# Kernel optimization log

Measured on AMD Instinct MI355X. Metric: run time of the kernel, lower is better.

## Reference

```python
import jax, jax.numpy as jnp
import numpy as np

EPS = 1e-5  # torch LayerNorm default

def layernorm(x, gamma, beta):
    mu = jnp.mean(x, axis=-1, keepdims=True)
    var = jnp.mean(jnp.square(x - mu), axis=-1, keepdims=True)
    return (x - mu) * jax.lax.rsqrt(var + EPS) * gamma + beta

def setup_inputs() -> dict:
    key = jax.random.key(0)
    ks = jax.random.split(key, 8)
    B, S, D = 4, 2048, 1024
    s = 1.0 / np.sqrt(D)  # torch Linear init scale
    return {
        "x": jax.random.normal(ks[0], (B, S, D), dtype=jnp.float32),
        "Wq": jax.random.uniform(ks[1], (D, D), jnp.float32, -s, s),
        "bq": jax.random.uniform(ks[2], (D,), jnp.float32, -s, s),
        "Wk": jax.random.uniform(ks[3], (D, D), jnp.float32, -s, s),
        "bk": jax.random.uniform(ks[4], (D,), jnp.float32, -s, s),
        "Wv": jax.random.uniform(ks[5], (D, D), jnp.float32, -s, s),
        "bv": jax.random.uniform(ks[6], (D,), jnp.float32, -s, s),
        "gamma": jnp.ones((D,), jnp.float32),
        "beta": jnp.zeros((D,), jnp.float32),
    }

def reference(x, Wq, bq, Wk, bk, Wv, bv, gamma, beta):
    # torch Linear: x @ W.T + b; shared LayerNorm applied to each projection
    q = layernorm(jnp.einsum('bsd,ed->bse', x, Wq) + bq, gamma, beta)
    k = layernorm(jnp.einsum('bsd,ed->bse', x, Wk) + bk, gamma, beta)
    v = layernorm(jnp.einsum('bsd,ed->bse', x, Wv) + bv, gamma, beta)
    att = jnp.einsum('bqd,bkd->bqk', q, k)  # no 1/sqrt(d) scaling in original
    att = jax.nn.softmax(att, axis=-1)
    # dropout is identity in eval mode (reference baseline)
    return jnp.einsum('bqk,bkd->bqd', att, v)
```

## Files before the change

kernel.cpp:

```cpp
#include <hip/hip_runtime.h>

typedef _Float16 f16;
typedef __attribute__((ext_vector_type(4))) _Float16 f16x4;
typedef __attribute__((ext_vector_type(8))) _Float16 f16x8;
typedef __attribute__((ext_vector_type(4))) float f32x4;

#define GLB_AS __attribute__((address_space(1)))
#define LDS_AS __attribute__((address_space(3)))

__device__ __forceinline__ void async_copy16(const void* g, void* l) {
  __builtin_amdgcn_global_load_lds((const GLB_AS void*)g, (LDS_AS void*)l, 16, 0, 0);
}

template <typename OutT, int MODE, bool BIAS>
__global__ __launch_bounds__(256) void gemm_kn(
    const f16* __restrict__ A, const f16* __restrict__ B, OutT* __restrict__ C,
    int lda, int ldb, int ldc, int K, long sA, long sB, long sC,
    int tiles_x, int tiles_y,
    const float* __restrict__ b0, const float* __restrict__ b1,
    const float* __restrict__ b2)
{
  constexpr int BM = 128, BK = 32;
  __shared__ __align__(16) f16 Ash[2][BM * BK];
  __shared__ __align__(16) f16 Bsh[2][BM * BK];

  int bx, by, bz;
  {
    const int n = blockIdx.x;
    if (MODE == 0) {
      by = n % tiles_y;
      const int r = n / tiles_y;
      bx = r % tiles_x;
      bz = r / tiles_x;
    } else {
      const int j = n & 7, i = n >> 3;
      bz = j >> 1;
      bx = i >> 3;
      by = (j & 1) * 8 + (i & 7);
    }
  }

  A += (long)bz * sA;
  B += (long)bz * sB;
  C += (long)bz * sC;

  const int tid  = threadIdx.x;
  const int wave = tid >> 6, lane = tid & 63;
  const int m0 = by * BM, n0 = bx * BM;
  const int wm = (wave >> 1) * 64, wn = (wave & 1) * 64;
  const int r16 = lane & 15, quad = lane >> 4;

  const int srow = wave * 32 + (lane >> 2);
  const int skb  = (lane & 3) * 8;
  const f16* Ag = A + (long)(m0 + srow) * lda + skb;
  const f16* Bg = B + (long)(n0 + srow) * ldb + skb;
  const int lo0 = (wave * 32) * BK;
  const int lo1 = (wave * 32 + 16) * BK;

  async_copy16(Ag,                  &Ash[0][lo0]);
  async_copy16(Ag + 16 * (long)lda, &Ash[0][lo1]);
  async_copy16(Bg,                  &Bsh[0][lo0]);
  async_copy16(Bg + 16 * (long)ldb, &Bsh[0][lo1]);

  f32x4 acc[4][4] = {};

  int buf = 0;
  for (int k0 = 0; k0 < K; k0 += BK, buf ^= 1) {
    __syncthreads();

    if (k0 + BK < K) {
      const int nb = buf ^ 1;
      const long k1 = k0 + BK;
      async_copy16(Ag + k1,                  &Ash[nb][lo0]);
      async_copy16(Ag + k1 + 16 * (long)lda, &Ash[nb][lo1]);
      async_copy16(Bg + k1,                  &Bsh[nb][lo0]);
      async_copy16(Bg + k1 + 16 * (long)ldb, &Bsh[nb][lo1]);
    }

    f16x8 af[4], bf[4];
#pragma unroll
    for (int i = 0; i < 4; i++) {
      af[i] = *(const f16x8*)&Ash[buf][(wm + i * 16 + r16) * BK + quad * 8];
      bf[i] = *(const f16x8*)&Bsh[buf][(wn + i * 16 + r16) * BK + quad * 8];
    }
#pragma unroll
    for (int i = 0; i < 4; i++)
#pragma unroll
      for (int j = 0; j < 4; j++)
        acc[i][j] = __builtin_amdgcn_mfma_f32_16x16x32_f16(af[i], bf[j], acc[i][j], 0, 0, 0);
  }

  float bias_j[4] = {0.f, 0.f, 0.f, 0.f};
  if (BIAS) {
    const float* bias = (bz == 0) ? b0 : (bz == 1) ? b1 : b2;
#pragma unroll
    for (int j = 0; j < 4; j++) bias_j[j] = bias[n0 + wn + j * 16 + r16];
  }
#pragma unroll
  for (int i = 0; i < 4; i++)
#pragma unroll
    for (int j = 0; j < 4; j++)
#pragma unroll
      for (int r = 0; r < 4; r++) {
        long row = m0 + wm + i * 16 + quad * 4 + r;
        long col = n0 + wn + j * 16 + r16;
        C[row * (long)ldc + col] = (OutT)(acc[i][j][r] + bias_j[j]);
      }
}

__global__ __launch_bounds__(256) void cast_all(
    const float* __restrict__ x, const float* __restrict__ Wq,
    const float* __restrict__ Wk, const float* __restrict__ Wv,
    f16* __restrict__ Xh, f16* __restrict__ Wh)
{
  const long off = (long)blockIdx.x * 1024 + threadIdx.x * 4;
  const float* src;
  f16* dst;
  if (off < 8388608L) {
    src = x + off;
    dst = Xh + off;
  } else {
    const long o = off - 8388608L;
    src = (o < 1048576L) ? Wq + o
        : (o < 2097152L) ? Wk + (o - 1048576L)
                         : Wv + (o - 2097152L);
    dst = Wh + o;
  }
  const float4 v = *(const float4*)src;
  f16x4 h;
  h.x = (f16)v.x; h.y = (f16)v.y; h.z = (f16)v.z; h.w = (f16)v.w;
  *(f16x4*)dst = h;
}

__global__ __launch_bounds__(256) void ln_kernel(
    f16* __restrict__ P, const float* __restrict__ gamma,
    const float* __restrict__ beta)
{
  f16* p = P + (long)blockIdx.y * 8388608 + (long)blockIdx.x * 1024;
  const int tid = threadIdx.x;
  const int e = tid * 4;

  f16x4 raw = *(const f16x4*)(p + e);
  float v0 = (float)raw.x, v1 = (float)raw.y;
  float v2 = (float)raw.z, v3 = (float)raw.w;
  float s  = v0 + v1 + v2 + v3;
  float s2 = v0 * v0 + v1 * v1 + v2 * v2 + v3 * v3;

#pragma unroll
  for (int off = 32; off > 0; off >>= 1) {
    s  += __shfl_down(s, off, 64);
    s2 += __shfl_down(s2, off, 64);
  }
  __shared__ float red[10];
  const int wave = tid >> 6, lane = tid & 63;
  if (lane == 0) { red[wave] = s; red[4 + wave] = s2; }
  __syncthreads();
  if (tid == 0) {
    red[8] = red[0] + red[1] + red[2] + red[3];
    red[9] = red[4] + red[5] + red[6] + red[7];
  }
  __syncthreads();
  const float mu   = red[8] * (1.f / 1024.f);
  const float var  = red[9] * (1.f / 1024.f) - mu * mu;
  const float rstd = rsqrtf(var + 1e-5f);

  float4 gg = *(const float4*)(gamma + e);
  float4 be = *(const float4*)(beta + e);
  f16x4 o;
  o.x = (f16)((v0 - mu) * rstd * gg.x + be.x);
  o.y = (f16)((v1 - mu) * rstd * gg.y + be.y);
  o.z = (f16)((v2 - mu) * rstd * gg.z + be.z);
  o.w = (f16)((v3 - mu) * rstd * gg.w + be.w);
  *(f16x4*)(p + e) = o;
}

__global__ __launch_bounds__(256) void transpose_kernel(const f16* __restrict__ V,
                                                        f16* __restrict__ Vt)
{
  const int S = 2048, D = 1024;
  const f16* v = V + (long)blockIdx.z * ((long)S * D);
  f16* vt = Vt + (long)blockIdx.z * ((long)D * S);
  __shared__ f16 tile[64][66];
  const int d0 = blockIdx.x * 64, j0 = blockIdx.y * 64;
  const int tx = threadIdx.x & 63, ty = threadIdx.x >> 6;
#pragma unroll
  for (int r = ty; r < 64; r += 4)
    tile[r][tx] = v[(long)(j0 + r) * D + d0 + tx];
  __syncthreads();
#pragma unroll
  for (int r = ty; r < 64; r += 4)
    vt[(long)(d0 + r) * S + j0 + tx] = tile[tx][r];
}

__global__ __launch_bounds__(256) void softmax_kernel(float* __restrict__ Sc)
{
  float* srow = Sc + (long)blockIdx.x * 2048;
  const int tid = threadIdx.x;
  float4 a = ((const float4*)srow)[tid];
  float4 b = ((const float4*)srow)[256 + tid];

  float m = fmaxf(fmaxf(fmaxf(a.x, a.y), fmaxf(a.z, a.w)),
                  fmaxf(fmaxf(b.x, b.y), fmaxf(b.z, b.w)));
#pragma unroll
  for (int off = 32; off > 0; off >>= 1) m = fmaxf(m, __shfl_down(m, off, 64));
  __shared__ float red[6];
  const int wave = tid >> 6, lane = tid & 63;
  if (lane == 0) red[wave] = m;
  __syncthreads();
  if (tid == 0) red[4] = fmaxf(fmaxf(red[0], red[1]), fmaxf(red[2], red[3]));
  __syncthreads();
  const float M = red[4];

  a.x = __expf(a.x - M); a.y = __expf(a.y - M);
  a.z = __expf(a.z - M); a.w = __expf(a.w - M);
  b.x = __expf(b.x - M); b.y = __expf(b.y - M);
  b.z = __expf(b.z - M); b.w = __expf(b.w - M);
  float s = a.x + a.y + a.z + a.w + b.x + b.y + b.z + b.w;
#pragma unroll
  for (int off = 32; off > 0; off >>= 1) s += __shfl_down(s, off, 64);
  if (lane == 0) red[wave] = s;
  __syncthreads();
  if (tid == 0) red[5] = red[0] + red[1] + red[2] + red[3];
  __syncthreads();
  const float inv = 1.0f / red[5];

  f16* orow = (f16*)srow;
  f16x4 oa, ob;
  oa.x = (f16)(a.x * inv); oa.y = (f16)(a.y * inv);
  oa.z = (f16)(a.z * inv); oa.w = (f16)(a.w * inv);
  ob.x = (f16)(b.x * inv); ob.y = (f16)(b.y * inv);
  ob.z = (f16)(b.z * inv); ob.w = (f16)(b.w * inv);
  ((f16x4*)orow)[tid]       = oa;
  ((f16x4*)orow)[256 + tid] = ob;
}

extern "C" void kernel_launch(void* const* d_in, const int* in_sizes, int n_in,
                              void* d_out, int out_size, void* d_ws, size_t ws_size,
                              hipStream_t stream)
{
  const float* x     = (const float*)d_in[0];
  const float* Wq    = (const float*)d_in[1];
  const float* bq    = (const float*)d_in[2];
  const float* Wk    = (const float*)d_in[3];
  const float* bk    = (const float*)d_in[4];
  const float* Wv    = (const float*)d_in[5];
  const float* bv    = (const float*)d_in[6];
  const float* gamma = (const float*)d_in[7];
  const float* beta  = (const float*)d_in[8];
  float* out = (float*)d_out;

  char* ws = (char*)d_ws;
  f16*   P  = (f16*)(ws);
  f16*   Vt = (f16*)(ws + (48u << 20));
  float* Sc = (float*)(ws + (64u << 20));
  f16*   Xh = (f16*)(ws + (64u << 20));
  f16*   Wh = (f16*)(ws + (80u << 20));

  cast_all<<<11264, 256, 0, stream>>>(x, Wq, Wk, Wv, Xh, Wh);

  gemm_kn<f16, 0, true><<<1536, 256, 0, stream>>>(
      Xh, Wh, P, 1024, 1024, 1024, 1024, 0L, 1048576L, 8388608L,
      8, 64, bq, bk, bv);

  ln_kernel<<<dim3(8192, 3), 256, 0, stream>>>(P, gamma, beta);

  transpose_kernel<<<dim3(16, 32, 4), 256, 0, stream>>>(P + 2L * 8388608, Vt);

  gemm_kn<float, 1, false><<<1024, 256, 0, stream>>>(
      P, P + 8388608, Sc, 1024, 1024, 2048, 1024, 2097152L, 2097152L, 4194304L,
      16, 16, nullptr, nullptr, nullptr);

  softmax_kernel<<<8192, 256, 0, stream>>>(Sc);

  gemm_kn<float, 1, false><<<512, 256, 0, stream>>>(
      (const f16*)Sc, Vt, out, 4096, 2048, 1024, 2048, 8388608L, 2097152L, 2097152L,
      8, 16, nullptr, nullptr, nullptr);
}
```

Before: 315.5 us.

## Replace GEMM with 8-wave, 4-stage pipelined kernel using larger tiles and swizzled LDS

Replaces the 256-thread, double-buffered 128x128 GEMM with a 512-thread kernel that uses 128x256 or 256x256 tiles. It keeps a 4-deep async global-to-LDS pipeline with explicit vmcnt waits, XOR-swizzles the LDS chunks to avoid bank conflicts, and splits each k-step into two halves. Each half interleaves the next stage's loads with the MFMA work under setprio and sched barriers. The aim is to hide global load latency, raise data reuse per tile and cut LDS conflicts in all three GEMMs. In exchange there are far fewer blocks per GEMM (256 for two of them), more LDS and register pressure, and hand-tuned waitcnt logic that is easy to get wrong.

New measurement: 305.0 us. 3.3% less time.

```diff
diff --git a/kernel.cpp b/kernel.cpp
--- a/kernel.cpp
+++ b/kernel.cpp
@@ -12,17 +12,38 @@
   __builtin_amdgcn_global_load_lds((const GLB_AS void*)g, (LDS_AS void*)l, 16, 0, 0);
 }
 
-template <typename OutT, int MODE, bool BIAS>
-__global__ __launch_bounds__(256) void gemm_kn(
+#define WAITVM(N) asm volatile("s_waitcnt vmcnt(" #N ")" ::: "memory")
+#define WAITLGKM0() asm volatile("s_waitcnt lgkmcnt(0)" ::: "memory")
+
+#define STAGE_A(t_) do {                                                     \
+    const int _b = (t_) & 3; const long _k = (long)(t_) * 32;                \
+    async_copy16(Ag + _k, &Ash[_b][sl]);                                     \
+    if constexpr (IA == 2)                                                   \
+      async_copy16(Ag + _k + 128l * lda, &Ash[_b][sl + 128 * 32]);           \
+  } while (0)
+#define STAGE_B(t_) do {                                                     \
+    const int _b = (t_) & 3; const long _k = (long)(t_) * 32;                \
+    async_copy16(Bg + _k, &Bsh[_b][sl]);                                     \
+    if constexpr (IB == 2)                                                   \
+      async_copy16(Bg + _k + 128l * ldb, &Bsh[_b][sl + 128 * 32]);           \
+  } while (0)
+
+template <int BM, int BN, typename OutT, int MODE, bool BIAS>
+__global__ __launch_bounds__(512, 2) void gemm8p(
     const f16* __restrict__ A, const f16* __restrict__ B, OutT* __restrict__ C,
     int lda, int ldb, int ldc, int K, long sA, long sB, long sC,
     int tiles_x, int tiles_y,
     const float* __restrict__ b0, const float* __restrict__ b1,
     const float* __restrict__ b2)
 {
-  constexpr int BM = 128, BK = 32;
-  __shared__ __align__(16) f16 Ash[2][BM * BK];
-  __shared__ __align__(16) f16 Bsh[2][BM * BK];
+  constexpr int BK = 32;
+  constexpr int WM = BM / 2, WN = BN / 4;
+  constexpr int RM = WM / 16, RN = WN / 16;
+  constexpr int IA = BM / 128, IB = BN / 128;
+  constexpr int IT = IA + IB;
+
+  __shared__ __align__(16) f16 Ash[4][BM * BK];
+  __shared__ __align__(16) f16 Bsh[4][BN * BK];
 
   int bx, by, bz;
   {
@@ -33,10 +54,10 @@
       bx = r % tiles_x;
       bz = r / tiles_x;
     } else {
-      const int j = n & 7, i = n >> 3;
+      const int j = n & 7, i = n >> 3, th = tiles_y >> 1;
       bz = j >> 1;
-      bx = i >> 3;
-      by = (j & 1) * 8 + (i & 7);
+      bx = i / th;
+      by = (j & 1) * th + i % th;
     }
   }
 
@@ -46,64 +67,124 @@
 
   const int tid  = threadIdx.x;
   const int wave = tid >> 6, lane = tid & 63;
-  const int m0 = by * BM, n0 = bx * BM;
-  const int wm = (wave >> 1) * 64, wn = (wave & 1) * 64;
+  const int wr = wave >> 2, wc = wave & 3;
+  const int m0 = by * BM, n0 = bx * BN;
   const int r16 = lane & 15, quad = lane >> 4;
 
-  const int srow = wave * 32 + (lane >> 2);
-  const int skb  = (lane & 3) * 8;
-  const f16* Ag = A + (long)(m0 + srow) * lda + skb;
-  const f16* Bg = B + (long)(n0 + srow) * ldb + skb;
-  const int lo0 = (wave * 32) * BK;
-  const int lo1 = (wave * 32 + 16) * BK;
-
-  async_copy16(Ag,                  &Ash[0][lo0]);
-  async_copy16(Ag + 16 * (long)lda, &Ash[0][lo1]);
-  async_copy16(Bg,                  &Bsh[0][lo0]);
-  async_copy16(Bg + 16 * (long)ldb, &Bsh[0][lo1]);
-
-  f32x4 acc[4][4] = {};
-
-  int buf = 0;
-  for (int k0 = 0; k0 < K; k0 += BK, buf ^= 1) {
-    __syncthreads();
-
-    if (k0 + BK < K) {
-      const int nb = buf ^ 1;
-      const long k1 = k0 + BK;
-      async_copy16(Ag + k1,                  &Ash[nb][lo0]);
-      async_copy16(Ag + k1 + 16 * (long)lda, &Ash[nb][lo1]);
-      async_copy16(Bg + k1,                  &Bsh[nb][lo0]);
-      async_copy16(Bg + k1 + 16 * (long)ldb, &Bsh[nb][lo1]);
+  const int srow = wave * 16 + (lane >> 2);
+  const int schunk = ((lane & 3) ^ ((lane >> 3) & 3)) * 8;
+  const f16* Ag = A + (long)(m0 + srow) * lda + schunk;
+  const f16* Bg = B + (long)(n0 + srow) * ldb + schunk;
+  const int sl = (wave * 16) * BK;
+
+  const int NT = K / BK;
+
+  STAGE_A(0); STAGE_B(0);
+  STAGE_A(1); STAGE_B(1);
+  STAGE_A(2); STAGE_B(2);
+
+  f32x4 acc[RM][RN] = {};
+
+  const int rchunk = (quad ^ ((r16 >> 1) & 3)) * 8;
+  const int rdA = (wr * WM + r16) * BK + rchunk;
+  const int rdB = (wc * WN + r16) * BK + rchunk;
+
+  for (int t = 0; t < NT; ++t) {
+    if constexpr (IT == 4) {
+      if (t < NT - 2) { WAITVM(8); } else if (t == NT - 2) { WAITVM(4); } else { WAITVM(0); }
+    } else {
+      if (t < NT - 2) { WAITVM(6); } else if (t == NT - 2) { WAITVM(3); } else { WAITVM(0); }
     }
-
-    f16x8 af[4], bf[4];
-#pragma unroll
-    for (int i = 0; i < 4; i++) {
-      af[i] = *(const f16x8*)&Ash[buf][(wm + i * 16 + r16) * BK + quad * 8];
-      bf[i] = *(const f16x8*)&Bsh[buf][(wn + i * 16 + r16) * BK + quad * 8];
+    __builtin_amdgcn_s_barrier();
+
+    const f16* As = Ash[t & 3];
+    const f16* Bs = Bsh[t & 3];
+    f16x8 af[4], bf[RN];
+
+    if constexpr (RM == 8) {
+#pragma unroll
+      for (int j = 0; j < RN; j++) bf[j] = *(const f16x8*)&Bs[rdB + j * 16 * BK];
+#pragma unroll
+      for (int i = 0; i < 4; i++) af[i] = *(const f16x8*)&As[rdA + i * 16 * BK];
+      if (t + 3 < NT) STAGE_A(t + 3);
+      __builtin_amdgcn_s_barrier();
+      WAITLGKM0();
+      __builtin_amdgcn_sched_barrier(0);
+      __builtin_amdgcn_s_setprio(1);
+#pragma unroll
+      for (int i = 0; i < 4; i++)
+#pragma unroll
+        for (int j = 0; j < RN; j++)
+          acc[i][j] = __builtin_amdgcn_mfma_f32_16x16x32_f16(af[i], bf[j], acc[i][j], 0, 0, 0);
+      __builtin_amdgcn_s_setprio(0);
+      __builtin_amdgcn_sched_barrier(0);
+      __builtin_amdgcn_s_barrier();
+      f16x8 af1[4];
+#pragma unroll
+      for (int i = 0; i < 4; i++) af1[i] = *(const f16x8*)&As[rdA + (4 + i) * 16 * BK];
+      if (t + 3 < NT) STAGE_B(t + 3);
+      __builtin_amdgcn_s_barrier();
+      WAITLGKM0();
+      __builtin_amdgcn_sched_barrier(0);
+      __builtin_amdgcn_s_setprio(1);
+#pragma unroll
+      for (int i = 0; i < 4; i++)
+#pragma unroll
+        for (int j = 0; j < RN; j++)
+          acc[4 + i][j] = __builtin_amdgcn_mfma_f32_16x16x32_f16(af1[i], bf[j], acc[4 + i][j], 0, 0, 0);
+      __builtin_amdgcn_s_setprio(0);
+      __builtin_amdgcn_sched_barrier(0);
+    } else {
+#pragma unroll
+      for (int i = 0; i < 4; i++) af[i] = *(const f16x8*)&As[rdA + i * 16 * BK];
+#pragma unroll
+      for (int j = 0; j < 2; j++) bf[j] = *(const f16x8*)&Bs[rdB + j * 16 * BK];
+      if (t + 3 < NT) STAGE_A(t + 3);
+      __builtin_amdgcn_s_barrier();
+      WAITLGKM0();
+      __builtin_amdgcn_sched_barrier(0);
+      __builtin_amdgcn_s_setprio(1);
+#pragma unroll
+      for (int i = 0; i < 4; i++)
+#pragma unroll
+        for (int j = 0; j < 2; j++)
+          acc[i][j] = __builtin_amdgcn_mfma_f32_16x16x32_f16(af[i], bf[j], acc[i][j], 0, 0, 0);
+      __builtin_amdgcn_s_setprio(0);
+      __builtin_amdgcn_sched_barrier(0);
+      __builtin_amdgcn_s_barrier();
+#pragma unroll
+      for (int j = 2; j < 4; j++) bf[j] = *(const f16x8*)&Bs[rdB + j * 16 * BK];
+      if (t + 3 < NT) STAGE_B(t + 3);
+      __builtin_amdgcn_s_barrier();
+      WAITLGKM0();
+      __builtin_amdgcn_sched_barrier(0);
+      __builtin_amdgcn_s_setprio(1);
+#pragma unroll
+      for (int i = 0; i < 4; i++)
+#pragma unroll
+        for (int j = 2; j < 4; j++)
+          acc[i][j] = __builtin_amdgcn_mfma_f32_16x16x32_f16(af[i], bf[j], acc[i][j], 0, 0, 0);
+      __builtin_amdgcn_s_setprio(0);
+      __builtin_amdgcn_sched_barrier(0);
     }
-#pragma unroll
-    for (int i = 0; i < 4; i++)
-#pragma unroll
-      for (int j = 0; j < 4; j++)
-        acc[i][j] = __builtin_amdgcn_mfma_f32_16x16x32_f16(af[i], bf[j], acc[i][j], 0, 0, 0);
-  }
-
-  float bias_j[4] = {0.f, 0.f, 0.f, 0.f};
-  if (BIAS) {
+  }
+
+  float bias_j[RN];
+#pragma unroll
+  for (int j = 0; j < RN; j++) bias_j[j] = 0.f;
+  if constexpr (BIAS) {
     const float* bias = (bz == 0) ? b0 : (bz == 1) ? b1 : b2;
 #pragma unroll
-    for (int j = 0; j < 4; j++) bias_j[j] = bias[n0 + wn + j * 16 + r16];
-  }
-#pragma unroll
-  for (int i = 0; i < 4; i++)
-#pragma unroll
-    for (int j = 0; j < 4; j++)
+    for (int j = 0; j < RN; j++) bias_j[j] = bias[n0 + wc * WN + j * 16 + r16];
+  }
+#pragma unroll
+  for (int i = 0; i < RM; i++)
+#pragma unroll
+    for (int j = 0; j < RN; j++)
 #pragma unroll
       for (int r = 0; r < 4; r++) {
-        long row = m0 + wm + i * 16 + quad * 4 + r;
-        long col = n0 + wn + j * 16 + r16;
+        long row = m0 + wr * WM + i * 16 + quad * 4 + r;
+        long col = n0 + wc * WN + j * 16 + r16;
         C[row * (long)ldc + col] = (OutT)(acc[i][j][r] + bias_j[j]);
       }
 }
@@ -258,21 +339,21 @@
 
   cast_all<<<11264, 256, 0, stream>>>(x, Wq, Wk, Wv, Xh, Wh);
 
-  gemm_kn<f16, 0, true><<<1536, 256, 0, stream>>>(
+  gemm8p<128, 256, f16, 0, true><<<768, 512, 0, stream>>>(
       Xh, Wh, P, 1024, 1024, 1024, 1024, 0L, 1048576L, 8388608L,
-      8, 64, bq, bk, bv);
+      4, 64, bq, bk, bv);
 
   ln_kernel<<<dim3(8192, 3), 256, 0, stream>>>(P, gamma, beta);
 
   transpose_kernel<<<dim3(16, 32, 4), 256, 0, stream>>>(P + 2L * 8388608, Vt);
 
-  gemm_kn<float, 1, false><<<1024, 256, 0, stream>>>(
+  gemm8p<256, 256, float, 1, false><<<256, 512, 0, stream>>>(
       P, P + 8388608, Sc, 1024, 1024, 2048, 1024, 2097152L, 2097152L, 4194304L,
-      16, 16, nullptr, nullptr, nullptr);
+      8, 8, nullptr, nullptr, nullptr);
 
   softmax_kernel<<<8192, 256, 0, stream>>>(Sc);
 
-  gemm_kn<float, 1, false><<<512, 256, 0, stream>>>(
+  gemm8p<128, 256, float, 1, false><<<256, 512, 0, stream>>>(
       (const f16*)Sc, Vt, out, 4096, 2048, 1024, 2048, 8388608L, 2097152L, 2097152L,
-      8, 16, nullptr, nullptr, nullptr);
-}
+      4, 16, nullptr, nullptr, nullptr);
+}
```

## Replace GEMM with larger-tile 4-stage pipelined kernel using swizzled LDS

Applied to the files above, without the earlier changes.

Replaces the 128x128 double-buffered GEMM with a templated 512-thread kernel using 128x256 or 256x256 tiles. It adds a four-deep async global-to-LDS pipeline with explicit vmcnt waits and raw barriers, and XOR-swizzles the LDS layout to cut bank conflicts. The goals are more data reuse per block and better hiding of load latency. The trade-off is more LDS per block and fewer blocks in the grid, which may underfill the GPU for the smaller GEMMs.

Measured after the change: 340.3 us. 7.8% more time.

```diff
diff --git a/kernel.cpp b/kernel.cpp
--- a/kernel.cpp
+++ b/kernel.cpp
@@ -12,17 +12,36 @@
   __builtin_amdgcn_global_load_lds((const GLB_AS void*)g, (LDS_AS void*)l, 16, 0, 0);
 }
 
-template <typename OutT, int MODE, bool BIAS>
-__global__ __launch_bounds__(256) void gemm_kn(
+#define WAITVM(N) asm volatile("s_waitcnt vmcnt(" #N ")" ::: "memory")
+#define BAR() __builtin_amdgcn_s_barrier()
+#define SB0() __builtin_amdgcn_sched_barrier(0)
+
+#define STAGE(g_) do {                                                       \
+    const long _k = (long)(g_) * 32;                                         \
+    f16* _da = &Ash[(g_) & 3][w16 * 32];                                     \
+    async_copy16(Ag + _k, _da);                                              \
+    if constexpr (IA == 2) async_copy16(Ag + _k + 128l * lda, _da + 4096);   \
+    f16* _db = &Bsh[(g_) & 3][w16 * 32];                                     \
+    async_copy16(Bg + _k, _db);                                              \
+    async_copy16(Bg + _k + 128l * ldb, _db + 4096);                          \
+  } while (0)
+
+template <int BM, int BN, typename OutT, int MODE, bool BIAS>
+__global__ __launch_bounds__(512, 2) void gemmc(
     const f16* __restrict__ A, const f16* __restrict__ B, OutT* __restrict__ C,
     int lda, int ldb, int ldc, int K, long sA, long sB, long sC,
     int tiles_x, int tiles_y,
     const float* __restrict__ b0, const float* __restrict__ b1,
     const float* __restrict__ b2)
 {
-  constexpr int BM = 128, BK = 32;
-  __shared__ __align__(16) f16 Ash[2][BM * BK];
-  __shared__ __align__(16) f16 Bsh[2][BM * BK];
+  constexpr int WM = BM / 2, WN = BN / 4;
+  constexpr int RM = WM / 16, RN = WN / 16;
+  constexpr int IA = BM / 128;
+  constexpr int IT = IA + 2;
+  static_assert(RN == 4 && BN == 256, "template assumes BN=256");
+
+  __shared__ __align__(16) f16 Ash[4][BM * 32];
+  __shared__ __align__(16) f16 Bsh[4][BN * 32];
 
   int bx, by, bz;
   {
@@ -33,10 +52,10 @@
       bx = r % tiles_x;
       bz = r / tiles_x;
     } else {
-      const int j = n & 7, i = n >> 3;
+      const int j = n & 7, i = n >> 3, th = tiles_y >> 1;
       bz = j >> 1;
-      bx = i >> 3;
-      by = (j & 1) * 8 + (i & 7);
+      bx = i / th;
+      by = (j & 1) * th + i % th;
     }
   }
 
@@ -46,64 +65,68 @@
 
   const int tid  = threadIdx.x;
   const int wave = tid >> 6, lane = tid & 63;
-  const int m0 = by * BM, n0 = bx * BM;
-  const int wm = (wave >> 1) * 64, wn = (wave & 1) * 64;
+  const int wr = wave >> 2, wc = wave & 3;
+  const int m0 = by * BM, n0 = bx * BN;
   const int r16 = lane & 15, quad = lane >> 4;
-
-  const int srow = wave * 32 + (lane >> 2);
-  const int skb  = (lane & 3) * 8;
-  const f16* Ag = A + (long)(m0 + srow) * lda + skb;
-  const f16* Bg = B + (long)(n0 + srow) * ldb + skb;
-  const int lo0 = (wave * 32) * BK;
-  const int lo1 = (wave * 32 + 16) * BK;
-
-  async_copy16(Ag,                  &Ash[0][lo0]);
-  async_copy16(Ag + 16 * (long)lda, &Ash[0][lo1]);
-  async_copy16(Bg,                  &Bsh[0][lo0]);
-  async_copy16(Bg + 16 * (long)ldb, &Bsh[0][lo1]);
-
-  f32x4 acc[4][4] = {};
-
-  int buf = 0;
-  for (int k0 = 0; k0 < K; k0 += BK, buf ^= 1) {
-    __syncthreads();
-
-    if (k0 + BK < K) {
-      const int nb = buf ^ 1;
-      const long k1 = k0 + BK;
-      async_copy16(Ag + k1,                  &Ash[nb][lo0]);
-      async_copy16(Ag + k1 + 16 * (long)lda, &Ash[nb][lo1]);
-      async_copy16(Bg + k1,                  &Bsh[nb][lo0]);
-      async_copy16(Bg + k1 + 16 * (long)ldb, &Bsh[nb][lo1]);
-    }
-
-    f16x8 af[4], bf[4];
-#pragma unroll
-    for (int i = 0; i < 4; i++) {
-      af[i] = *(const f16x8*)&Ash[buf][(wm + i * 16 + r16) * BK + quad * 8];
-      bf[i] = *(const f16x8*)&Bsh[buf][(wn + i * 16 + r16) * BK + quad * 8];
-    }
-#pragma unroll
-    for (int i = 0; i < 4; i++)
+  const int w16 = wave * 16;
+
+  const int cg8 = (((lane & 3) ^ ((lane >> 3) & 3)) * 8);
+  const f16* Ag = A + (long)(m0 + w16 + (lane >> 2)) * lda + cg8;
+  const f16* Bg = B + (long)(n0 + w16 + (lane >> 2)) * ldb + cg8;
+
+  const int NG = K / 32;
+
+  STAGE(0); STAGE(1); STAGE(2);
+
+  f32x4 acc[RM][RN] = {};
+
+  const int rc  = (quad ^ ((r16 >> 1) & 3)) * 8;
+  const int rdA = (wr * WM + r16) * 32 + rc;
+  const int rdB = (wc * WN + r16) * 32 + rc;
+
+  if constexpr (IT == 3) { WAITVM(6); } else { WAITVM(8); }
+  BAR(); SB0();
+
+  for (int g = 0; g < NG; ++g) {
+    if (g + 3 < NG) STAGE(g + 3);
+
+    const f16* As = Ash[g & 3];
+    const f16* Bs = Bsh[g & 3];
+    f16x8 af[RM], bf[4];
+#pragma unroll
+    for (int j = 0; j < 4; j++) bf[j] = *(const f16x8*)&Bs[rdB + j * 512];
+#pragma unroll
+    for (int i = 0; i < RM; i++) af[i] = *(const f16x8*)&As[rdA + i * 512];
+#pragma unroll
+    for (int i = 0; i < RM; i++)
 #pragma unroll
       for (int j = 0; j < 4; j++)
         acc[i][j] = __builtin_amdgcn_mfma_f32_16x16x32_f16(af[i], bf[j], acc[i][j], 0, 0, 0);
-  }
-
-  float bias_j[4] = {0.f, 0.f, 0.f, 0.f};
-  if (BIAS) {
+
+    if (g < NG - 1) {
+      if (g <= NG - 4) { if constexpr (IT == 3) { WAITVM(6); } else { WAITVM(8); } }
+      else if (g == NG - 3) { if constexpr (IT == 3) { WAITVM(3); } else { WAITVM(4); } }
+      else { WAITVM(0); }
+      BAR(); SB0();
+    }
+  }
+
+  float bias_j[RN];
+#pragma unroll
+  for (int j = 0; j < RN; j++) bias_j[j] = 0.f;
+  if constexpr (BIAS) {
     const float* bias = (bz == 0) ? b0 : (bz == 1) ? b1 : b2;
 #pragma unroll
-    for (int j = 0; j < 4; j++) bias_j[j] = bias[n0 + wn + j * 16 + r16];
-  }
-#pragma unroll
-  for (int i = 0; i < 4; i++)
-#pragma unroll
-    for (int j = 0; j < 4; j++)
+    for (int j = 0; j < RN; j++) bias_j[j] = bias[n0 + wc * WN + j * 16 + r16];
+  }
+#pragma unroll
+  for (int i = 0; i < RM; i++)
+#pragma unroll
+    for (int j = 0; j < RN; j++)
 #pragma unroll
       for (int r = 0; r < 4; r++) {
-        long row = m0 + wm + i * 16 + quad * 4 + r;
-        long col = n0 + wn + j * 16 + r16;
+        long row = m0 + wr * WM + i * 16 + quad * 4 + r;
+        long col = n0 + wc * WN + j * 16 + r16;
         C[row * (long)ldc + col] = (OutT)(acc[i][j][r] + bias_j[j]);
       }
 }
@@ -258,21 +281,21 @@
 
   cast_all<<<11264, 256, 0, stream>>>(x, Wq, Wk, Wv, Xh, Wh);
 
-  gemm_kn<f16, 0, true><<<1536, 256, 0, stream>>>(
+  gemmc<128, 256, f16, 0, true><<<768, 512, 0, stream>>>(
       Xh, Wh, P, 1024, 1024, 1024, 1024, 0L, 1048576L, 8388608L,
-      8, 64, bq, bk, bv);
+      4, 64, bq, bk, bv);
 
   ln_kernel<<<dim3(8192, 3), 256, 0, stream>>>(P, gamma, beta);
 
   transpose_kernel<<<dim3(16, 32, 4), 256, 0, stream>>>(P + 2L * 8388608, Vt);
 
-  gemm_kn<float, 1, false><<<1024, 256, 0, stream>>>(
+  gemmc<256, 256, float, 1, false><<<256, 512, 0, stream>>>(
       P, P + 8388608, Sc, 1024, 1024, 2048, 1024, 2097152L, 2097152L, 4194304L,
-      16, 16, nullptr, nullptr, nullptr);
+      8, 8, nullptr, nullptr, nullptr);
 
   softmax_kernel<<<8192, 256, 0, stream>>>(Sc);
 
-  gemm_kn<float, 1, false><<<512, 256, 0, stream>>>(
+  gemmc<128, 256, float, 1, false><<<256, 512, 0, stream>>>(
       (const f16*)Sc, Vt, out, 4096, 2048, 1024, 2048, 8388608L, 2097152L, 2097152L,
-      8, 16, nullptr, nullptr, nullptr);
-}
+      4, 16, nullptr, nullptr, nullptr);
+}
```
